# Performance work log

Hardware: AMD Instinct MI355X
Metric: run time of the kernel (lower is better)

## Reference

```python
import jax, jax.numpy as jnp
import numpy as np

EMB_DIM = 128
HIDDEN = 1024
CL_TEMPERATURE = 0.5
NUM_LABELS = 20
EPS = 1e-14


def setup_inputs() -> dict:
    key = jax.random.key(0)
    k1, k2, k3, k4, k5, k6 = jax.random.split(key, 6)
    B, L = 4, 128
    token_repr = jax.random.normal(k1, (B, L, HIDDEN), dtype=jnp.float32)
    labels = jax.random.randint(k2, (B, L), 0, NUM_LABELS, dtype=jnp.int64)
    mask = jnp.ones((B, L), dtype=jnp.int64)
    # Linear params (PyTorch default init scale ~ U(-1/sqrt(fan_in), 1/sqrt(fan_in)))
    s = 1.0 / np.sqrt(HIDDEN)
    W_mu = jax.random.uniform(k3, (HIDDEN, EMB_DIM), jnp.float32, -s, s)
    b_mu = jax.random.uniform(k4, (EMB_DIM,), jnp.float32, -s, s)
    W_sigma = jax.random.uniform(k5, (HIDDEN, EMB_DIM), jnp.float32, -s, s)
    b_sigma = jax.random.uniform(k6, (EMB_DIM,), jnp.float32, -s, s)
    return {"token_repr": token_repr, "labels": labels, "mask": mask,
            "W_mu": W_mu, "b_mu": b_mu, "W_sigma": W_sigma, "b_sigma": b_sigma}


def _pairwise_sym_kl(mu, sigma):
    """Symmetric diagonal-Gaussian KL between all pairs. mu,sigma: [N,D] -> [N,N]."""
    D = mu.shape[-1]
    mu_i, mu_j = mu[:, None, :], mu[None, :, :]          # [N,N,D] broadcast
    si, sj = sigma[:, None, :], sigma[None, :, :]
    r_ij = sj / si                                        # [N,N,D]
    ij_kl = 0.5 * (r_ij.sum(-1)
                   + (((mu_i - mu_j) ** 2) / si).sum(-1)
                   - D
                   - jnp.log(r_ij + EPS).sum(-1))
    r_ji = si / sj
    ji_kl = 0.5 * (r_ji.sum(-1)
                   + (((mu_j - mu_i) ** 2) / sj).sum(-1)
                   - D
                   - jnp.log(r_ji + EPS).sum(-1))
    return 0.5 * (ij_kl + ji_kl)


def reference(token_repr, labels, mask, W_mu, b_mu, W_sigma, b_sigma):
    h = jax.nn.relu(token_repr)                           # nn.ReLU before Linear
    mu = (h @ W_mu + b_mu).reshape(-1, EMB_DIM)           # [N,D]
    sigma = (jax.nn.elu(h @ W_sigma + b_sigma) + 1.0 + EPS).reshape(-1, EMB_DIM)
    lab = labels.reshape(-1)
    valid = (mask.reshape(-1) == 1) & (lab > 0)           # torch does this by filtering; we mask

    # loss = -symmetric KL for all pairs (cl_type='kl')
    loss = -_pairwise_sym_kl(mu, sigma)                   # [N,N]

    # denominator mask: all embedding dims differ (excludes self / duplicates)
    all_diff = jnp.all(mu[:, None, :] != mu[None, :, :], axis=-1)
    den_mask = all_diff & valid[:, None] & valid[None, :]
    num_mask = den_mask & (lab[:, None] == lab[None, :])

    # NT-Xent with masked reduction; rows with zero positives (or invalid) dropped
    e = jnp.exp(loss / CL_TEMPERATURE)                    # kl >= 0 so e <= 1, stable
    cnts = jnp.sum(num_mask, axis=1).astype(loss.dtype)
    loss_num = jnp.sum(e * num_mask, axis=1)
    loss_den = jnp.sum(e * den_mask, axis=1)
    include = cnts > 0
    safe = lambda x: jnp.where(include, x, 1.0)
    loss_final = -jnp.log(safe(loss_num)) + jnp.log(safe(loss_den)) + jnp.log(safe(cnts))
    n_inc = jnp.maximum(jnp.sum(include), 1).astype(loss.dtype)
    return jnp.sum(jnp.where(include, loss_final, 0.0)) / n_inc
```

## Files before the change

kernel.cpp:

```cpp
#include <hip/hip_runtime.h>
#include <math.h>

#define N_TOK 512
#define DIM   128
#define KDIM  1024
#define EPSF  1e-14f

__global__ __launch_bounds__(512) void proj_part(
    const float* __restrict__ token, const float* __restrict__ Wmu,
    const float* __restrict__ Wsg, float* __restrict__ part)
{
    __shared__ float hs[32][128];
    const int bid = blockIdx.x;
    const int ng = bid >> 4, cs = (bid >> 3) & 1, ks = bid & 7;
    const int t = threadIdx.x;

    #pragma unroll
    for (int rep = 0; rep < 2; ++rep) {
        int f = t + rep * 512;
        int row = f >> 5, kq = f & 31;
        float4 v = *(const float4*)(token + (size_t)(ng * 32 + row) * KDIM + ks * 128 + kq * 4);
        v.x = fmaxf(v.x, 0.f); v.y = fmaxf(v.y, 0.f);
        v.z = fmaxf(v.z, 0.f); v.w = fmaxf(v.w, 0.f);
        *(float4*)(&hs[row][kq * 4]) = v;
    }
    __syncthreads();

    const int q = t & 31;
    const int rsub = t >> 5;
    const float* __restrict__ W = (cs ? Wsg : Wmu) + (size_t)(ks * 128) * DIM + q * 4;

    float4 a0 = make_float4(0.f, 0.f, 0.f, 0.f);
    float4 a1 = make_float4(0.f, 0.f, 0.f, 0.f);
    #pragma unroll 2
    for (int k4 = 0; k4 < 32; ++k4) {
        float4 h0 = *(const float4*)(&hs[rsub][k4 * 4]);
        float4 h1 = *(const float4*)(&hs[rsub + 16][k4 * 4]);
        const float* wp = W + (size_t)(k4 * 4) * DIM;
        float4 w0 = *(const float4*)(wp);
        float4 w1 = *(const float4*)(wp + DIM);
        float4 w2 = *(const float4*)(wp + 2 * DIM);
        float4 w3 = *(const float4*)(wp + 3 * DIM);
        a0.x = fmaf(h0.x, w0.x, a0.x); a0.y = fmaf(h0.x, w0.y, a0.y);
        a0.z = fmaf(h0.x, w0.z, a0.z); a0.w = fmaf(h0.x, w0.w, a0.w);
        a0.x = fmaf(h0.y, w1.x, a0.x); a0.y = fmaf(h0.y, w1.y, a0.y);
        a0.z = fmaf(h0.y, w1.z, a0.z); a0.w = fmaf(h0.y, w1.w, a0.w);
        a0.x = fmaf(h0.z, w2.x, a0.x); a0.y = fmaf(h0.z, w2.y, a0.y);
        a0.z = fmaf(h0.z, w2.z, a0.z); a0.w = fmaf(h0.z, w2.w, a0.w);
        a0.x = fmaf(h0.w, w3.x, a0.x); a0.y = fmaf(h0.w, w3.y, a0.y);
        a0.z = fmaf(h0.w, w3.z, a0.z); a0.w = fmaf(h0.w, w3.w, a0.w);
        a1.x = fmaf(h1.x, w0.x, a1.x); a1.y = fmaf(h1.x, w0.y, a1.y);
        a1.z = fmaf(h1.x, w0.z, a1.z); a1.w = fmaf(h1.x, w0.w, a1.w);
        a1.x = fmaf(h1.y, w1.x, a1.x); a1.y = fmaf(h1.y, w1.y, a1.y);
        a1.z = fmaf(h1.y, w1.z, a1.z); a1.w = fmaf(h1.y, w1.w, a1.w);
        a1.x = fmaf(h1.z, w2.x, a1.x); a1.y = fmaf(h1.z, w2.y, a1.y);
        a1.z = fmaf(h1.z, w2.z, a1.z); a1.w = fmaf(h1.z, w2.w, a1.w);
        a1.x = fmaf(h1.w, w3.x, a1.x); a1.y = fmaf(h1.w, w3.y, a1.y);
        a1.z = fmaf(h1.w, w3.z, a1.z); a1.w = fmaf(h1.w, w3.w, a1.w);
    }
    const int r0 = ng * 32 + rsub;
    float* dst = part + ((size_t)ks * N_TOK + r0) * 256 + cs * 128 + q * 4;
    *(float4*)dst = a0;
    *(float4*)(dst + 16 * 256) = a1;
}

__global__ __launch_bounds__(256) void proj_finish(
    const float* __restrict__ part, const float* __restrict__ bmu,
    const float* __restrict__ bsg,
    float* __restrict__ mu, float* __restrict__ sg, float* __restrict__ iv)
{
    const int rg = blockIdx.x;
    const int t = threadIdx.x;
    const int q = t & 31, r = t >> 5;
    const int row = rg * 8 + r;
    const int d = q * 4;

    float4 sm = make_float4(0.f, 0.f, 0.f, 0.f);
    float4 ss = make_float4(0.f, 0.f, 0.f, 0.f);
    #pragma unroll
    for (int ks = 0; ks < 8; ++ks) {
        const float* base = part + ((size_t)ks * N_TOK + row) * 256;
        float4 v0 = *(const float4*)(base + d);
        float4 v1 = *(const float4*)(base + 128 + d);
        sm.x += v0.x; sm.y += v0.y; sm.z += v0.z; sm.w += v0.w;
        ss.x += v1.x; ss.y += v1.y; ss.z += v1.z; ss.w += v1.w;
    }
    {
        float4 b = *(const float4*)(bmu + d);
        sm.x += b.x; sm.y += b.y; sm.z += b.z; sm.w += b.w;
    }
    float4 e, vv;
    {
        float4 b = *(const float4*)(bsg + d);
        float x0 = ss.x + b.x, x1 = ss.y + b.y, x2 = ss.z + b.z, x3 = ss.w + b.w;
        e.x = (x0 > 0.f ? x0 : expm1f(x0)) + 1.0f + EPSF;
        e.y = (x1 > 0.f ? x1 : expm1f(x1)) + 1.0f + EPSF;
        e.z = (x2 > 0.f ? x2 : expm1f(x2)) + 1.0f + EPSF;
        e.w = (x3 > 0.f ? x3 : expm1f(x3)) + 1.0f + EPSF;
        vv.x = 1.0f / e.x; vv.y = 1.0f / e.y; vv.z = 1.0f / e.z; vv.w = 1.0f / e.w;
    }
    *(float4*)(mu + (size_t)row * DIM + d) = sm;
    *(float4*)(sg + (size_t)row * DIM + d) = e;
    *(float4*)(iv + (size_t)row * DIM + d) = vv;
}

__global__ __launch_bounds__(256) void pair_kernel(
    const float* __restrict__ mu, const float* __restrict__ sg,
    const float* __restrict__ iv, const int* __restrict__ labels,
    const int* __restrict__ mask, float* __restrict__ gpart)
{
    __shared__ float sj[3][DIM][33];
    __shared__ int slab[16], svalid[16];
    const int ig = blockIdx.x >> 4, jg = blockIdx.x & 15;
    const int i0 = ig * 16, j0 = jg * 32;
    const int t = threadIdx.x;

    {
        float* sjf = &sj[0][0][0];
        #pragma unroll
        for (int rep = 0; rep < 4; ++rep) {
            int rem = t + rep * 256;
            int row = rem >> 5, dq = rem & 31;
            size_t src = (size_t)(j0 + row) * DIM + dq * 4;
            int b = (dq * 4) * 33 + row;
            float4 v;
            v = *(const float4*)(mu + src);
            sjf[b] = v.x; sjf[b + 33] = v.y; sjf[b + 66] = v.z; sjf[b + 99] = v.w;
            v = *(const float4*)(sg + src);
            sjf[4224 + b] = v.x; sjf[4224 + b + 33] = v.y;
            sjf[4224 + b + 66] = v.z; sjf[4224 + b + 99] = v.w;
            v = *(const float4*)(iv + src);
            sjf[8448 + b] = v.x; sjf[8448 + b + 33] = v.y;
            sjf[8448 + b + 66] = v.z; sjf[8448 + b + 99] = v.w;
        }
    }
    if (t < 16) {
        int lab = labels[i0 + t];
        slab[t] = lab;
        svalid[t] = (mask[i0 + t] == 1 && lab > 0) ? 1 : 0;
    }
    __syncthreads();

    const int jl = t & 31, isub = t >> 5;
    const int ia = 2 * isub;
    const int j = j0 + jl;
    const int labj = labels[j];
    const bool validj = (mask[j] == 1) && (labj > 0);

    const float* pm = mu + (size_t)(i0 + ia) * DIM;
    const float* ps = sg + (size_t)(i0 + ia) * DIM;
    const float* pv = iv + (size_t)(i0 + ia) * DIM;

    float accA = 0.f, accB = 0.f;
    float mnA = 1e30f, mnB = 1e30f;

    #pragma unroll 4
    for (int q = 0; q < 32; ++q) {
        const int d0 = q * 4;
        float jm0 = sj[0][d0 + 0][jl], jm1 = sj[0][d0 + 1][jl];
        float jm2 = sj[0][d0 + 2][jl], jm3 = sj[0][d0 + 3][jl];
        float js0 = sj[1][d0 + 0][jl], js1 = sj[1][d0 + 1][jl];
        float js2 = sj[1][d0 + 2][jl], js3 = sj[1][d0 + 3][jl];
        float jv0 = sj[2][d0 + 0][jl], jv1 = sj[2][d0 + 1][jl];
        float jv2 = sj[2][d0 + 2][jl], jv3 = sj[2][d0 + 3][jl];

        float4 mA = *(const float4*)(pm + d0);
        float4 sA = *(const float4*)(ps + d0);
        float4 vA = *(const float4*)(pv + d0);
        float4 mB = *(const float4*)(pm + DIM + d0);
        float4 sB = *(const float4*)(ps + DIM + d0);
        float4 vB = *(const float4*)(pv + DIM + d0);

        float dm;
        dm = mA.x - jm0; accA = fmaf(fmaf(dm, dm, js0), vA.x, fmaf(fmaf(dm, dm, sA.x), jv0, accA)); mnA = fminf(mnA, fabsf(dm));
        dm = mA.y - jm1; accA = fmaf(fmaf(dm, dm, js1), vA.y, fmaf(fmaf(dm, dm, sA.y), jv1, accA)); mnA = fminf(mnA, fabsf(dm));
        dm = mA.z - jm2; accA = fmaf(fmaf(dm, dm, js2), vA.z, fmaf(fmaf(dm, dm, sA.z), jv2, accA)); mnA = fminf(mnA, fabsf(dm));
        dm = mA.w - jm3; accA = fmaf(fmaf(dm, dm, js3), vA.w, fmaf(fmaf(dm, dm, sA.w), jv3, accA)); mnA = fminf(mnA, fabsf(dm));

        dm = mB.x - jm0; accB = fmaf(fmaf(dm, dm, js0), vB.x, fmaf(fmaf(dm, dm, sB.x), jv0, accB)); mnB = fminf(mnB, fabsf(dm));
        dm = mB.y - jm1; accB = fmaf(fmaf(dm, dm, js1), vB.y, fmaf(fmaf(dm, dm, sB.y), jv1, accB)); mnB = fminf(mnB, fabsf(dm));
        dm = mB.z - jm2; accB = fmaf(fmaf(dm, dm, js2), vB.z, fmaf(fmaf(dm, dm, sB.z), jv2, accB)); mnB = fminf(mnB, fabsf(dm));
        dm = mB.w - jm3; accB = fmaf(fmaf(dm, dm, js3), vB.w, fmaf(fmaf(dm, dm, sB.w), jv3, accB)); mnB = fminf(mnB, fabsf(dm));
    }

    const int ib = ia + 1;
    float eA = expf(128.0f - 0.5f * accA);
    float eB = expf(128.0f - 0.5f * accB);
    bool pvA = validj && (svalid[ia] != 0) && (mnA != 0.0f);
    bool pvB = validj && (svalid[ib] != 0) && (mnB != 0.0f);
    bool smA = pvA && (labj == slab[ia]);
    bool smB = pvB && (labj == slab[ib]);
    float dA = pvA ? eA : 0.f, nA = smA ? eA : 0.f, cA = smA ? 1.f : 0.f;
    float dB = pvB ? eB : 0.f, nB = smB ? eB : 0.f, cB = smB ? 1.f : 0.f;

    #pragma unroll
    for (int m = 1; m < 32; m <<= 1) {
        cA += __shfl_xor(cA, m); nA += __shfl_xor(nA, m); dA += __shfl_xor(dA, m);
        cB += __shfl_xor(cB, m); nB += __shfl_xor(nB, m); dB += __shfl_xor(dB, m);
    }
    if (jl == 0) {
        float* pa = gpart + ((size_t)jg * N_TOK + i0 + ia) * 3;
        float* pb = gpart + ((size_t)jg * N_TOK + i0 + ib) * 3;
        pa[0] = cA; pa[1] = nA; pa[2] = dA;
        pb[0] = cB; pb[1] = nB; pb[2] = dB;
    }
}

__global__ __launch_bounds__(512) void final_kernel(
    const float* __restrict__ gpart, float* __restrict__ out)
{
    __shared__ float redL[8], redI[8];
    const int t = threadIdx.x;
    float c = 0.f, nm = 0.f, dn = 0.f;
    #pragma unroll
    for (int jg = 0; jg < 16; ++jg) {
        const float* p = gpart + ((size_t)jg * N_TOK + t) * 3;
        c += p[0]; nm += p[1]; dn += p[2];
    }
    const bool inc = c > 0.5f;
    float lf = inc ? (-logf(nm) + logf(dn) + logf(c)) : 0.f;
    float fi = inc ? 1.f : 0.f;
    #pragma unroll
    for (int m = 1; m < 64; m <<= 1) {
        lf += __shfl_xor(lf, m);
        fi += __shfl_xor(fi, m);
    }
    if ((t & 63) == 0) { redL[t >> 6] = lf; redI[t >> 6] = fi; }
    __syncthreads();
    if (t == 0) {
        float L = 0.f, I = 0.f;
        #pragma unroll
        for (int w = 0; w < 8; ++w) { L += redL[w]; I += redI[w]; }
        out[0] = L / fmaxf(I, 1.0f);
    }
}

extern "C" void kernel_launch(void* const* d_in, const int* in_sizes, int n_in,
                              void* d_out, int out_size, void* d_ws, size_t ws_size,
                              hipStream_t stream) {
    const float* token  = (const float*)d_in[0];
    const int*   labels = (const int*)d_in[1];
    const int*   mask   = (const int*)d_in[2];
    const float* Wmu    = (const float*)d_in[3];
    const float* bmu    = (const float*)d_in[4];
    const float* Wsg    = (const float*)d_in[5];
    const float* bsg    = (const float*)d_in[6];

    float* ws = (float*)d_ws;
    float* part  = ws;
    float* mu    = part + 1048576;
    float* sg    = mu + 65536;
    float* iv    = sg + 65536;
    float* gpart = iv + 65536;

    proj_part<<<256, 512, 0, stream>>>(token, Wmu, Wsg, part);
    proj_finish<<<64, 256, 0, stream>>>(part, bmu, bsg, mu, sg, iv);
    pair_kernel<<<512, 256, 0, stream>>>(mu, sg, iv, labels, mask, gpart);
    final_kernel<<<1, 512, 0, stream>>>(gpart, (float*)d_out);
}
```

Measured before the change: 101.1 us.

## Fuse projection split-K reduction in-block and merge final reduce into pair kernel

The projection kernel now does the whole K reduction inside one block, splitting K across four thread groups and combining them in shared memory. It then applies bias and ELU directly, so the partial-sum workspace and the proj_finish launch are gone. The final scalar reduction moves into the pair kernel as a last-block-done pattern using an atomic counter and threadfence, which removes another launch. The trade-off is that each block now loads a full 8x1024 token tile and reads W from global memory with less reuse across rows.

```diff
diff --git a/kernel.cpp b/kernel.cpp
--- a/kernel.cpp
+++ b/kernel.cpp
@@ -6,111 +6,98 @@
 #define KDIM  1024
 #define EPSF  1e-14f
 
-__global__ __launch_bounds__(512) void proj_part(
+__global__ __launch_bounds__(512) void proj_fused(
     const float* __restrict__ token, const float* __restrict__ Wmu,
-    const float* __restrict__ Wsg, float* __restrict__ part)
+    const float* __restrict__ bmu, const float* __restrict__ Wsg,
+    const float* __restrict__ bsg, float* __restrict__ mu,
+    float* __restrict__ sg, float* __restrict__ iv, int* __restrict__ done)
 {
-    __shared__ float hs[32][128];
+    __shared__ float hs[8][KDIM];
+    __shared__ float4 red[3][8][16];
     const int bid = blockIdx.x;
-    const int ng = bid >> 4, cs = (bid >> 3) & 1, ks = bid & 7;
     const int t = threadIdx.x;
-
-    #pragma unroll
-    for (int rep = 0; rep < 2; ++rep) {
-        int f = t + rep * 512;
-        int row = f >> 5, kq = f & 31;
-        float4 v = *(const float4*)(token + (size_t)(ng * 32 + row) * KDIM + ks * 128 + kq * 4);
-        v.x = fmaxf(v.x, 0.f); v.y = fmaxf(v.y, 0.f);
-        v.z = fmaxf(v.z, 0.f); v.w = fmaxf(v.w, 0.f);
-        *(float4*)(&hs[row][kq * 4]) = v;
-    }
-    __syncthreads();
-
-    const int q = t & 31;
-    const int rsub = t >> 5;
-    const float* __restrict__ W = (cs ? Wsg : Wmu) + (size_t)(ks * 128) * DIM + q * 4;
-
-    float4 a0 = make_float4(0.f, 0.f, 0.f, 0.f);
-    float4 a1 = make_float4(0.f, 0.f, 0.f, 0.f);
-    #pragma unroll 2
-    for (int k4 = 0; k4 < 32; ++k4) {
-        float4 h0 = *(const float4*)(&hs[rsub][k4 * 4]);
-        float4 h1 = *(const float4*)(&hs[rsub + 16][k4 * 4]);
+    if (bid == 0 && t == 0) *done = 0;
+
+    const int rowg = bid >> 2, colsel = bid & 3;
+    const int m = colsel >> 1, ch = colsel & 1;
+
+    {
+        const float4* src = (const float4*)(token + (size_t)rowg * 8 * KDIM);
+        float4* dst = (float4*)&hs[0][0];
+        #pragma unroll
+        for (int r = 0; r < 4; ++r) {
+            int idx = t + r * 512;
+            float4 v = src[idx];
+            v.x = fmaxf(v.x, 0.f); v.y = fmaxf(v.y, 0.f);
+            v.z = fmaxf(v.z, 0.f); v.w = fmaxf(v.w, 0.f);
+            dst[idx] = v;
+        }
+    }
+    __syncthreads();
+
+    const int q = t & 15, rsub = t >> 4;
+    const int row = rsub & 7, kq = rsub >> 3;
+    const int d = ch * 64 + q * 4;
+    const float* __restrict__ W = (m ? Wsg : Wmu) + (size_t)(kq * 256) * DIM + d;
+    const float4* hp = (const float4*)(&hs[row][kq * 256]);
+
+    float4 acc = make_float4(0.f, 0.f, 0.f, 0.f);
+    #pragma unroll 4
+    for (int k4 = 0; k4 < 64; ++k4) {
+        float4 h = hp[k4];
         const float* wp = W + (size_t)(k4 * 4) * DIM;
         float4 w0 = *(const float4*)(wp);
         float4 w1 = *(const float4*)(wp + DIM);
         float4 w2 = *(const float4*)(wp + 2 * DIM);
         float4 w3 = *(const float4*)(wp + 3 * DIM);
-        a0.x = fmaf(h0.x, w0.x, a0.x); a0.y = fmaf(h0.x, w0.y, a0.y);
-        a0.z = fmaf(h0.x, w0.z, a0.z); a0.w = fmaf(h0.x, w0.w, a0.w);
-        a0.x = fmaf(h0.y, w1.x, a0.x); a0.y = fmaf(h0.y, w1.y, a0.y);
-        a0.z = fmaf(h0.y, w1.z, a0.z); a0.w = fmaf(h0.y, w1.w, a0.w);
-        a0.x = fmaf(h0.z, w2.x, a0.x); a0.y = fmaf(h0.z, w2.y, a0.y);
-        a0.z = fmaf(h0.z, w2.z, a0.z); a0.w = fmaf(h0.z, w2.w, a0.w);
-        a0.x = fmaf(h0.w, w3.x, a0.x); a0.y = fmaf(h0.w, w3.y, a0.y);
-        a0.z = fmaf(h0.w, w3.z, a0.z); a0.w = fmaf(h0.w, w3.w, a0.w);
-        a1.x = fmaf(h1.x, w0.x, a1.x); a1.y = fmaf(h1.x, w0.y, a1.y);
-        a1.z = fmaf(h1.x, w0.z, a1.z); a1.w = fmaf(h1.x, w0.w, a1.w);
-        a1.x = fmaf(h1.y, w1.x, a1.x); a1.y = fmaf(h1.y, w1.y, a1.y);
-        a1.z = fmaf(h1.y, w1.z, a1.z); a1.w = fmaf(h1.y, w1.w, a1.w);
-        a1.x = fmaf(h1.z, w2.x, a1.x); a1.y = fmaf(h1.z, w2.y, a1.y);
-        a1.z = fmaf(h1.z, w2.z, a1.z); a1.w = fmaf(h1.z, w2.w, a1.w);
-        a1.x = fmaf(h1.w, w3.x, a1.x); a1.y = fmaf(h1.w, w3.y, a1.y);
-        a1.z = fmaf(h1.w, w3.z, a1.z); a1.w = fmaf(h1.w, w3.w, a1.w);
-    }
-    const int r0 = ng * 32 + rsub;
-    float* dst = part + ((size_t)ks * N_TOK + r0) * 256 + cs * 128 + q * 4;
-    *(float4*)dst = a0;
-    *(float4*)(dst + 16 * 256) = a1;
+        acc.x = fmaf(h.x, w0.x, acc.x); acc.y = fmaf(h.x, w0.y, acc.y);
+        acc.z = fmaf(h.x, w0.z, acc.z); acc.w = fmaf(h.x, w0.w, acc.w);
+        acc.x = fmaf(h.y, w1.x, acc.x); acc.y = fmaf(h.y, w1.y, acc.y);
+        acc.z = fmaf(h.y, w1.z, acc.z); acc.w = fmaf(h.y, w1.w, acc.w);
+        acc.x = fmaf(h.z, w2.x, acc.x); acc.y = fmaf(h.z, w2.y, acc.y);
+        acc.z = fmaf(h.z, w2.z, acc.z); acc.w = fmaf(h.z, w2.w, acc.w);
+        acc.x = fmaf(h.w, w3.x, acc.x); acc.y = fmaf(h.w, w3.y, acc.y);
+        acc.z = fmaf(h.w, w3.z, acc.z); acc.w = fmaf(h.w, w3.w, acc.w);
+    }
+
+    if (kq > 0) red[kq - 1][row][q] = acc;
+    __syncthreads();
+    if (kq == 0) {
+        float4 r0 = red[0][row][q], r1 = red[1][row][q], r2 = red[2][row][q];
+        acc.x += r0.x + r1.x + r2.x; acc.y += r0.y + r1.y + r2.y;
+        acc.z += r0.z + r1.z + r2.z; acc.w += r0.w + r1.w + r2.w;
+        const int rowi = rowg * 8 + row;
+        if (m == 0) {
+            float4 b = *(const float4*)(bmu + d);
+            acc.x += b.x; acc.y += b.y; acc.z += b.z; acc.w += b.w;
+            *(float4*)(mu + (size_t)rowi * DIM + d) = acc;
+        } else {
+            float4 b = *(const float4*)(bsg + d);
+            float x0 = acc.x + b.x, x1 = acc.y + b.y;
+            float x2 = acc.z + b.z, x3 = acc.w + b.w;
+            float4 e, vv;
+            e.x = (x0 > 0.f ? x0 : expm1f(x0)) + 1.0f + EPSF;
+            e.y = (x1 > 0.f ? x1 : expm1f(x1)) + 1.0f + EPSF;
+            e.z = (x2 > 0.f ? x2 : expm1f(x2)) + 1.0f + EPSF;
+            e.w = (x3 > 0.f ? x3 : expm1f(x3)) + 1.0f + EPSF;
+            vv.x = 1.0f / e.x; vv.y = 1.0f / e.y;
+            vv.z = 1.0f / e.z; vv.w = 1.0f / e.w;
+            *(float4*)(sg + (size_t)rowi * DIM + d) = e;
+            *(float4*)(iv + (size_t)rowi * DIM + d) = vv;
+        }
+    }
 }
 
-__global__ __launch_bounds__(256) void proj_finish(
-    const float* __restrict__ part, const float* __restrict__ bmu,
-    const float* __restrict__ bsg,
-    float* __restrict__ mu, float* __restrict__ sg, float* __restrict__ iv)
-{
-    const int rg = blockIdx.x;
-    const int t = threadIdx.x;
-    const int q = t & 31, r = t >> 5;
-    const int row = rg * 8 + r;
-    const int d = q * 4;
-
-    float4 sm = make_float4(0.f, 0.f, 0.f, 0.f);
-    float4 ss = make_float4(0.f, 0.f, 0.f, 0.f);
-    #pragma unroll
-    for (int ks = 0; ks < 8; ++ks) {
-        const float* base = part + ((size_t)ks * N_TOK + row) * 256;
-        float4 v0 = *(const float4*)(base + d);
-        float4 v1 = *(const float4*)(base + 128 + d);
-        sm.x += v0.x; sm.y += v0.y; sm.z += v0.z; sm.w += v0.w;
-        ss.x += v1.x; ss.y += v1.y; ss.z += v1.z; ss.w += v1.w;
-    }
-    {
-        float4 b = *(const float4*)(bmu + d);
-        sm.x += b.x; sm.y += b.y; sm.z += b.z; sm.w += b.w;
-    }
-    float4 e, vv;
-    {
-        float4 b = *(const float4*)(bsg + d);
-        float x0 = ss.x + b.x, x1 = ss.y + b.y, x2 = ss.z + b.z, x3 = ss.w + b.w;
-        e.x = (x0 > 0.f ? x0 : expm1f(x0)) + 1.0f + EPSF;
-        e.y = (x1 > 0.f ? x1 : expm1f(x1)) + 1.0f + EPSF;
-        e.z = (x2 > 0.f ? x2 : expm1f(x2)) + 1.0f + EPSF;
-        e.w = (x3 > 0.f ? x3 : expm1f(x3)) + 1.0f + EPSF;
-        vv.x = 1.0f / e.x; vv.y = 1.0f / e.y; vv.z = 1.0f / e.z; vv.w = 1.0f / e.w;
-    }
-    *(float4*)(mu + (size_t)row * DIM + d) = sm;
-    *(float4*)(sg + (size_t)row * DIM + d) = e;
-    *(float4*)(iv + (size_t)row * DIM + d) = vv;
-}
-
-__global__ __launch_bounds__(256) void pair_kernel(
+__global__ __launch_bounds__(256) void pair_final(
     const float* __restrict__ mu, const float* __restrict__ sg,
     const float* __restrict__ iv, const int* __restrict__ labels,
-    const int* __restrict__ mask, float* __restrict__ gpart)
+    const int* __restrict__ mask, float* __restrict__ gpart,
+    int* __restrict__ done, float* __restrict__ out)
 {
     __shared__ float sj[3][DIM][33];
     __shared__ int slab[16], svalid[16];
+    __shared__ int slast;
+    __shared__ float redL[4], redI[4];
     const int ig = blockIdx.x >> 4, jg = blockIdx.x & 15;
     const int i0 = ig * 16, j0 = jg * 32;
     const int t = threadIdx.x;
@@ -204,33 +191,38 @@
         pa[0] = cA; pa[1] = nA; pa[2] = dA;
         pb[0] = cB; pb[1] = nB; pb[2] = dB;
     }
-}
-
-__global__ __launch_bounds__(512) void final_kernel(
-    const float* __restrict__ gpart, float* __restrict__ out)
-{
-    __shared__ float redL[8], redI[8];
-    const int t = threadIdx.x;
-    float c = 0.f, nm = 0.f, dn = 0.f;
+
+    __threadfence();
+    if (t == 0) slast = (atomicAdd(done, 1) == 511);
+    __syncthreads();
+    if (!slast) return;
+    __threadfence();
+
+    float lfs = 0.f, fis = 0.f;
     #pragma unroll
-    for (int jg = 0; jg < 16; ++jg) {
-        const float* p = gpart + ((size_t)jg * N_TOK + t) * 3;
-        c += p[0]; nm += p[1]; dn += p[2];
-    }
-    const bool inc = c > 0.5f;
-    float lf = inc ? (-logf(nm) + logf(dn) + logf(c)) : 0.f;
-    float fi = inc ? 1.f : 0.f;
+    for (int rr = 0; rr < 2; ++rr) {
+        const int row = t + rr * 256;
+        float c = 0.f, nm = 0.f, dn = 0.f;
+        #pragma unroll
+        for (int g = 0; g < 16; ++g) {
+            const float* p = gpart + ((size_t)g * N_TOK + row) * 3;
+            c += p[0]; nm += p[1]; dn += p[2];
+        }
+        if (c > 0.5f) {
+            lfs += -logf(nm) + logf(dn) + logf(c);
+            fis += 1.f;
+        }
+    }
     #pragma unroll
     for (int m = 1; m < 64; m <<= 1) {
-        lf += __shfl_xor(lf, m);
-        fi += __shfl_xor(fi, m);
-    }
-    if ((t & 63) == 0) { redL[t >> 6] = lf; redI[t >> 6] = fi; }
+        lfs += __shfl_xor(lfs, m);
+        fis += __shfl_xor(fis, m);
+    }
+    if ((t & 63) == 0) { redL[t >> 6] = lfs; redI[t >> 6] = fis; }
     __syncthreads();
     if (t == 0) {
-        float L = 0.f, I = 0.f;
-        #pragma unroll
-        for (int w = 0; w < 8; ++w) { L += redL[w]; I += redI[w]; }
+        float L = redL[0] + redL[1] + redL[2] + redL[3];
+        float I = redI[0] + redI[1] + redI[2] + redI[3];
         out[0] = L / fmaxf(I, 1.0f);
     }
 }
@@ -247,14 +239,13 @@
     const float* bsg    = (const float*)d_in[6];
 
     float* ws = (float*)d_ws;
-    float* part  = ws;
-    float* mu    = part + 1048576;
+    float* mu    = ws;
     float* sg    = mu + 65536;
     float* iv    = sg + 65536;
     float* gpart = iv + 65536;
-
-    proj_part<<<256, 512, 0, stream>>>(token, Wmu, Wsg, part);
-    proj_finish<<<64, 256, 0, stream>>>(part, bmu, bsg, mu, sg, iv);
-    pair_kernel<<<512, 256, 0, stream>>>(mu, sg, iv, labels, mask, gpart);
-    final_kernel<<<1, 512, 0, stream>>>(gpart, (float*)d_out);
+    int*   done  = (int*)(gpart + 24576);
+
+    proj_fused<<<256, 512, 0, stream>>>(token, Wmu, bmu, Wsg, bsg, mu, sg, iv, done);
+    pair_final<<<512, 256, 0, stream>>>(mu, sg, iv, labels, mask, gpart, done,
+                                        (float*)d_out);
 }
```

Result: slower. 135.1 us (+33.6%).
